# Optimization experiments

Measured on AMD Instinct MI355X. Metric: run time of the kernel, lower is better.

## Reference

```python
import jax, jax.numpy as jnp
import numpy as np

D_MODEL = 512
N_HEADS = 8
D_HEAD = D_MODEL // N_HEADS
D_FF = 2048
LN_EPS = 1e-5


def _layer_norm(x, g, b):
    mu = jnp.mean(x, axis=-1, keepdims=True)
    var = jnp.var(x, axis=-1, keepdims=True)
    return (x - mu) * jax.lax.rsqrt(var + LN_EPS) * g + b


def setup_inputs() -> dict:
    key = jax.random.key(0)
    ks = jax.random.split(key, 16)
    s_d = 1.0 / np.sqrt(D_MODEL)
    s_f = 1.0 / np.sqrt(D_FF)
    x = jax.random.normal(ks[0], (32, 512, D_MODEL), dtype=jnp.float32)
    # per-head Q/K/V linears stacked over heads: [H, D, dh] weights, [H, dh] biases
    Wq = jax.random.uniform(ks[1], (N_HEADS, D_MODEL, D_HEAD), jnp.float32, -s_d, s_d)
    bq = jax.random.uniform(ks[2], (N_HEADS, D_HEAD), jnp.float32, -s_d, s_d)
    Wk = jax.random.uniform(ks[3], (N_HEADS, D_MODEL, D_HEAD), jnp.float32, -s_d, s_d)
    bk = jax.random.uniform(ks[4], (N_HEADS, D_HEAD), jnp.float32, -s_d, s_d)
    Wv = jax.random.uniform(ks[5], (N_HEADS, D_MODEL, D_HEAD), jnp.float32, -s_d, s_d)
    bv = jax.random.uniform(ks[6], (N_HEADS, D_HEAD), jnp.float32, -s_d, s_d)
    Wo = jax.random.uniform(ks[7], (D_MODEL, D_MODEL), jnp.float32, -s_d, s_d)
    bo = jax.random.uniform(ks[8], (D_MODEL,), jnp.float32, -s_d, s_d)
    ln1_g = jnp.ones((D_MODEL,), jnp.float32)
    ln1_b = jnp.zeros((D_MODEL,), jnp.float32)
    W1 = jax.random.uniform(ks[9], (D_MODEL, D_FF), jnp.float32, -s_d, s_d)
    b1 = jax.random.uniform(ks[10], (D_FF,), jnp.float32, -s_d, s_d)
    W2 = jax.random.uniform(ks[11], (D_FF, D_MODEL), jnp.float32, -s_f, s_f)
    b2 = jax.random.uniform(ks[12], (D_MODEL,), jnp.float32, -s_f, s_f)
    ln2_g = jnp.ones((D_MODEL,), jnp.float32)
    ln2_b = jnp.zeros((D_MODEL,), jnp.float32)
    return dict(x=x, Wq=Wq, bq=bq, Wk=Wk, bk=bk, Wv=Wv, bv=bv, Wo=Wo, bo=bo,
                ln1_g=ln1_g, ln1_b=ln1_b, W1=W1, b1=b1, W2=W2, b2=b2,
                ln2_g=ln2_g, ln2_b=ln2_b)


def reference(x, Wq, bq, Wk, bk, Wv, bv, Wo, bo, ln1_g, ln1_b, W1, b1, W2, b2, ln2_g, ln2_b):
    B, T, D = x.shape
    # batched-heads Q/K/V: [B, H, T, dh]
    q = jnp.einsum('btd,hde->bhte', x, Wq) + bq[None, :, None, :]
    k = jnp.einsum('btd,hde->bhte', x, Wk) + bk[None, :, None, :]
    v = jnp.einsum('btd,hde->bhte', x, Wv) + bv[None, :, None, :]
    scale = D_HEAD ** -0.5
    scores = jnp.einsum('bhte,bhse->bhts', q, k) * scale  # [B,H,T,T]
    causal = jnp.tril(jnp.ones((T, T), dtype=bool))
    scores = jnp.where(causal[None, None], scores, -jnp.inf)
    w = jax.nn.softmax(scores, axis=-1)
    o = jnp.einsum('bhts,bhse->bhte', w, v)              # [B,H,T,dh]
    o = jnp.transpose(o, (0, 2, 1, 3)).reshape(B, T, D)   # concat heads
    attn = o @ Wo + bo
    out1 = x + _layer_norm(attn, ln1_g, ln1_b)            # post-LN on sublayer output (as in source)
    ff = jax.nn.relu(out1 @ W1 + b1) @ W2 + b2
    return out1 + _layer_norm(ff, ln2_g, ln2_b)
```

## Files before the change

### kernel.cpp

```cpp
#include <hip/hip_runtime.h>
#include <hip/hip_bf16.h>


#define D_MODEL 512
#define N_HEADS 8
#define D_HEAD 64
#define D_FF 2048
#define NROWS 16384

typedef __bf16 bf16x8 __attribute__((ext_vector_type(8)));
typedef float f32x4 __attribute__((ext_vector_type(4)));
typedef float f32x16 __attribute__((ext_vector_type(16)));

#define SWZ(x) ((x) ^ ((((x) >> 7) & 7) << 4))

static __device__ __forceinline__ ushort f2bf(float f) {
    union { float f; unsigned u; } v; v.f = f;
    unsigned r = v.u + 0x7fffu + ((v.u >> 16) & 1u);
    return (ushort)(r >> 16);
}
static __device__ __forceinline__ unsigned pack2(float lo, float hi) {
    return (unsigned)f2bf(lo) | ((unsigned)f2bf(hi) << 16);
}
static __device__ __forceinline__ void async16(const void* g, void* l) {
    __builtin_amdgcn_global_load_lds(
        (const __attribute__((address_space(1))) void*)g,
        (__attribute__((address_space(3))) void*)l, 16, 0, 0);
}

__global__ __launch_bounds__(256) void conv_bf_kernel(
    const float* __restrict__ src, ushort* __restrict__ dst, int n8)
{
    int i = blockIdx.x * 256 + threadIdx.x;
    if (i >= n8) return;
    const float4* s = (const float4*)src;
    float4 a = s[i * 2], b = s[i * 2 + 1];
    uint4 o;
    o.x = pack2(a.x, a.y); o.y = pack2(a.z, a.w);
    o.z = pack2(b.x, b.y); o.w = pack2(b.z, b.w);
    ((uint4*)dst)[i] = o;
}

static __device__ __forceinline__ void tile_transpose_body(
    const float* __restrict__ src, int srcldc, ushort* __restrict__ dst, int Rd,
    int r0, int c0)
{
    __shared__ float t[64][65];
    int tid = threadIdx.x;
    int lr = tid >> 4, lc4 = (tid & 15) * 4;
    #pragma unroll
    for (int i = 0; i < 4; ++i) {
        float4 v = *(const float4*)&src[(size_t)(r0 + lr + i * 16) * srcldc + c0 + lc4];
        t[lr + i * 16][lc4 + 0] = v.x;
        t[lr + i * 16][lc4 + 1] = v.y;
        t[lr + i * 16][lc4 + 2] = v.z;
        t[lr + i * 16][lc4 + 3] = v.w;
    }
    __syncthreads();
    int oc = tid >> 2, orr = (tid & 3) * 16;
    uint4 u0, u1;
    u0.x = pack2(t[orr + 0][oc],  t[orr + 1][oc]);
    u0.y = pack2(t[orr + 2][oc],  t[orr + 3][oc]);
    u0.z = pack2(t[orr + 4][oc],  t[orr + 5][oc]);
    u0.w = pack2(t[orr + 6][oc],  t[orr + 7][oc]);
    u1.x = pack2(t[orr + 8][oc],  t[orr + 9][oc]);
    u1.y = pack2(t[orr + 10][oc], t[orr + 11][oc]);
    u1.z = pack2(t[orr + 12][oc], t[orr + 13][oc]);
    u1.w = pack2(t[orr + 14][oc], t[orr + 15][oc]);
    ushort* d = dst + (size_t)(c0 + oc) * Rd + r0 + orr;
    *(uint4*)&d[0] = u0;
    *(uint4*)&d[8] = u1;
}

__global__ __launch_bounds__(256) void transpose_bf_kernel(
    const float* __restrict__ src, ushort* __restrict__ dst, int R, int C)
{
    tile_transpose_body(src, C, dst, R, blockIdx.y * 64, blockIdx.x * 64);
}

__global__ __launch_bounds__(256) void qkv_pack_kernel(
    const float* __restrict__ Wq, const float* __restrict__ Wk,
    const float* __restrict__ Wv, ushort* __restrict__ WpT)
{
    int z = blockIdx.z;
    int p = z >> 3, h = z & 7;
    const float* src = ((p == 0) ? Wq : (p == 1) ? Wk : Wv) + (size_t)h * D_MODEL * D_HEAD;
    ushort* dst = WpT + (size_t)(p * D_MODEL + h * D_HEAD) * D_MODEL;
    tile_transpose_body(src, D_HEAD, dst, D_MODEL, blockIdx.y * 64, 0);
}

__global__ __launch_bounds__(256) void pack_bias_kernel(
    const float* __restrict__ bq, const float* __restrict__ bk,
    const float* __restrict__ bv, float* __restrict__ bp)
{
    int idx = blockIdx.x * 256 + threadIdx.x;
    if (idx >= 3 * D_MODEL) return;
    int p = idx / D_MODEL;
    int h = (idx % D_MODEL) / D_HEAD;
    int e = idx % D_HEAD;
    const float* bb = (p == 0) ? bq : (p == 1) ? bk : bv;
    bp[idx] = bb[h * D_HEAD + e];
}

template<int OMODE, bool RELU>
__global__ __launch_bounds__(512, 1) void gemm_bf16_kernel(
    const ushort* __restrict__ A, const ushort* __restrict__ BT,
    const float* __restrict__ bias, void* __restrict__ Cout,
    ushort* __restrict__ Qg, ushort* __restrict__ Kg, ushort* __restrict__ Vt,
    int M, int N, int K, int nbx)
{
    extern __shared__ __align__(16) char smem[];

    const int tid = threadIdx.x;
    const int wid = tid >> 6, l = tid & 63;
    const int wr = wid >> 1, wc = wid & 1;

    const int total = gridDim.x;
    const int cpx = total >> 3;
    const int flat = blockIdx.x;
    const int swz = (flat & 7) * cpx + (flat >> 3);
    const int bx = swz % nbx, by = swz / nbx;
    const int m0 = by * 256, n0 = bx * 128;

    const int srow = tid >> 3;
    const int sbyte = (tid & 7) * 16;
    const int ssw = sbyte ^ ((srow & 7) << 4);

    #define STAGE(t)                                                          \
    {                                                                         \
        const int kk_ = (t) * 64;                                             \
        char* dst_ = smem + ((t) & 1) * 49152;                                \
        _Pragma("unroll")                                                     \
        for (int i = 0; i < 4; ++i)                                           \
            async16((const char*)(A + (size_t)(m0 + i * 64 + srow) * K + kk_) \
                        + ssw,                                                \
                    dst_ + i * 8192 + tid * 16);                              \
        _Pragma("unroll")                                                     \
        for (int i = 0; i < 2; ++i)                                           \
            async16((const char*)(BT + (size_t)(n0 + i * 64 + srow) * K + kk_)\
                        + ssw,                                                \
                    dst_ + 32768 + i * 8192 + tid * 16);                      \
    }

    const int fl = l & 31, fh = l >> 5;
    const int frsw = (fl & 7) << 4;

    f32x16 acc[2][2] = {};

    STAGE(0);
    const int T = K >> 6;
    for (int t = 0; t < T; ++t) {
        __builtin_amdgcn_s_barrier();
        if (t + 1 < T) {
            STAGE(t + 1);
            asm volatile("s_waitcnt vmcnt(6)" ::: "memory");
        } else {
            asm volatile("s_waitcnt vmcnt(0)" ::: "memory");
        }
        __builtin_amdgcn_sched_barrier(0);

        const char* bufA = smem + (t & 1) * 49152;
        const char* bufB = bufA + 32768;
        #pragma unroll
        for (int ks = 0; ks < 4; ++ks) {
            const int kb = ((ks * 32 + fh * 16) ^ frsw);
            bf16x8 af[2], bfv[2];
            #pragma unroll
            for (int mi = 0; mi < 2; ++mi)
                af[mi] = *(const bf16x8*)(bufA +
                    (wr * 64 + mi * 32 + fl) * 128 + kb);
            #pragma unroll
            for (int ni = 0; ni < 2; ++ni)
                bfv[ni] = *(const bf16x8*)(bufB +
                    (wc * 64 + ni * 32 + fl) * 128 + kb);
            #pragma unroll
            for (int mi = 0; mi < 2; ++mi)
                #pragma unroll
                for (int ni = 0; ni < 2; ++ni)
                    acc[mi][ni] = __builtin_amdgcn_mfma_f32_32x32x16_bf16(
                        af[mi], bfv[ni], acc[mi][ni], 0, 0, 0);
        }
    }

    #pragma unroll
    for (int ni = 0; ni < 2; ++ni) {
        const int c = n0 + wc * 64 + ni * 32 + fl;
        const float bvv = bias ? bias[c] : 0.f;
        #pragma unroll
        for (int mi = 0; mi < 2; ++mi) {
            const int rbase = m0 + wr * 64 + mi * 32 + (fh << 2);
            float vv[16];
            #pragma unroll
            for (int reg = 0; reg < 16; ++reg) {
                float v = acc[mi][ni][reg] + bvv;
                if (RELU) v = fmaxf(v, 0.f);
                vv[reg] = v;
            }
            if (OMODE == 0) {
                #pragma unroll
                for (int reg = 0; reg < 16; ++reg) {
                    int r = rbase + (reg & 3) + ((reg >> 2) << 3);
                    ((float*)Cout)[(size_t)r * N + c] = vv[reg];
                }
            } else if (OMODE == 1) {
                #pragma unroll
                for (int reg = 0; reg < 16; ++reg) {
                    int r = rbase + (reg & 3) + ((reg >> 2) << 3);
                    ((ushort*)Cout)[(size_t)r * N + c] = f2bf(vv[reg]);
                }
            } else {
                const int p = n0 >> 9;
                const int h = (c >> 6) & 7, e = c & 63;
                #pragma unroll
                for (int q = 0; q < 4; ++q) {
                    int r0 = rbase + (q << 3);
                    int b = r0 >> 9, t0 = r0 & 511;
                    size_t bh = (size_t)(b * 8 + h);
                    if (p == 2) {
                        uint2 pk;
                        pk.x = pack2(vv[q * 4 + 0], vv[q * 4 + 1]);
                        pk.y = pack2(vv[q * 4 + 2], vv[q * 4 + 3]);
                        *(uint2*)&Vt[bh * 32768 + (size_t)e * 512 + t0] = pk;
                    } else {
                        ushort* dst = (p == 0 ? Qg : Kg) + bh * 32768 +
                                      (size_t)t0 * 64 + e;
                        dst[0]   = f2bf(vv[q * 4 + 0]);
                        dst[64]  = f2bf(vv[q * 4 + 1]);
                        dst[128] = f2bf(vv[q * 4 + 2]);
                        dst[192] = f2bf(vv[q * 4 + 3]);
                    }
                }
            }
        }
    }
    #undef STAGE
}

__global__ __launch_bounds__(256) void attn_kernel(
    const ushort* __restrict__ Qg,
    const ushort* __restrict__ Kg,
    const ushort* __restrict__ Vt,
    ushort* __restrict__ O)
{
    __shared__ __align__(16) char QP[8192];
    __shared__ __align__(16) char KB[2][8192];
    __shared__ __align__(16) char VB[2][8192];

    const int bh = blockIdx.x, qb = blockIdx.y;
    const int tid = threadIdx.x;
    const int w = tid >> 6, l = tid & 63;

    const ushort* Qb = Qg + (size_t)bh * 32768;
    const ushort* Kb = Kg + (size_t)bh * 32768;
    const ushort* Vb = Vt + (size_t)bh * 32768;

    #pragma unroll
    for (int i = 0; i < 2; ++i) {
        int Xi = i * 4096 + tid * 16;
        int row = Xi >> 7;
        int sw = SWZ(Xi) & 127;
        async16((const char*)(Qb + (size_t)(qb * 64 + row) * 64) + sw, QP + Xi);
    }
    #define STAGEKV(kt, bb)                                                     \
        { _Pragma("unroll")                                                     \
          for (int i = 0; i < 2; ++i) {                                         \
              int Xi = i * 4096 + tid * 16;                                     \
              int row = Xi >> 7;                                                \
              int sw = SWZ(Xi) & 127;                                           \
              async16((const char*)(Kb + (size_t)((kt) * 64 + row) * 64) + sw,  \
                      KB[bb] + Xi);                                             \
              async16((const char*)(Vb + (size_t)row * 512 + (kt) * 64) + sw,   \
                      VB[bb] + Xi);                                             \
          } }
    STAGEKV(0, 0);
    __syncthreads();

    bf16x8 qf[2];
    {
        int qrow = w * 16 + (l & 15);
        #pragma unroll
        for (int ks = 0; ks < 2; ++ks) {
            int X = qrow * 128 + ks * 64 + (l >> 4) * 16;
            qf[ks] = *(const bf16x8*)(QP + SWZ(X));
        }
    }

    float mrow = -INFINITY, lrow = 0.f;
    f32x4 oacc[4] = {};

    for (int kt = 0; kt <= qb; ++kt) {
        int cur = kt & 1;
        if (kt < qb) STAGEKV(kt + 1, cur ^ 1);

        f32x4 sacc[4] = {};
        #pragma unroll
        for (int ks = 0; ks < 2; ++ks) {
            #pragma unroll
            for (int mi = 0; mi < 4; ++mi) {
                int X = (mi * 16 + (l & 15)) * 128 + ks * 64 + (l >> 4) * 16;
                bf16x8 kf = *(const bf16x8*)(KB[cur] + SWZ(X));
                sacc[mi] = __builtin_amdgcn_mfma_f32_16x16x32_bf16(
                    kf, qf[ks], sacc[mi], 0, 0, 0);
            }
        }

        float sv[16];
        float tmax = -INFINITY;
        const int qrow_t = w * 16 + (l & 15);
        #pragma unroll
        for (int mi = 0; mi < 4; ++mi)
            #pragma unroll
            for (int r = 0; r < 4; ++r) {
                float s = sacc[mi][r] * 0.125f;
                if (kt == qb) {
                    int key_l = mi * 16 + (l >> 4) * 4 + r;
                    if (key_l > qrow_t) s = -INFINITY;
                }
                sv[mi * 4 + r] = s;
                tmax = fmaxf(tmax, s);
            }
        tmax = fmaxf(tmax, __shfl_xor(tmax, 16));
        tmax = fmaxf(tmax, __shfl_xor(tmax, 32));
        float mnew = fmaxf(mrow, tmax);
        float corr = __expf(mrow - mnew);
        mrow = mnew;
        float psum = 0.f;
        #pragma unroll
        for (int i = 0; i < 16; ++i) { sv[i] = __expf(sv[i] - mnew); psum += sv[i]; }
        psum += __shfl_xor(psum, 16);
        psum += __shfl_xor(psum, 32);
        lrow = lrow * corr + psum;

        #pragma unroll
        for (int mi = 0; mi < 4; ++mi) {
            uint2 pk;
            pk.x = pack2(sv[mi * 4 + 0], sv[mi * 4 + 1]);
            pk.y = pack2(sv[mi * 4 + 2], sv[mi * 4 + 3]);
            int X = qrow_t * 128 + (mi * 16 + (l >> 4) * 4) * 2;
            *(uint2*)(QP + SWZ(X)) = pk;
        }

        #pragma unroll
        for (int r = 0; r < 4; ++r) {
            float cr = __shfl(corr, (l & 48) | ((l >> 4) * 4 + r));
            #pragma unroll
            for (int n = 0; n < 4; ++n) oacc[n][r] *= cr;
        }

        #pragma unroll
        for (int ks = 0; ks < 2; ++ks) {
            int Xa = qrow_t * 128 + ks * 64 + (l >> 4) * 16;
            bf16x8 pa = *(const bf16x8*)(QP + SWZ(Xa));
            #pragma unroll
            for (int n = 0; n < 4; ++n) {
                int Xb = (n * 16 + (l & 15)) * 128 + ks * 64 + (l >> 4) * 16;
                bf16x8 vb = *(const bf16x8*)(VB[cur] + SWZ(Xb));
                oacc[n] = __builtin_amdgcn_mfma_f32_16x16x32_bf16(
                    pa, vb, oacc[n], 0, 0, 0);
            }
        }
        __syncthreads();
    }

    float linv = 1.0f / lrow;
    const int b_ = bh >> 3, h_ = bh & 7;
    #pragma unroll
    for (int r = 0; r < 4; ++r) {
        float li = __shfl(linv, (l & 48) | ((l >> 4) * 4 + r));
        int trow = qb * 64 + w * 16 + (l >> 4) * 4 + r;
        size_t obase = ((size_t)b_ * 512 + trow) * 512 + h_ * 64 + (l & 15);
        #pragma unroll
        for (int n = 0; n < 4; ++n)
            O[obase + n * 16] = f2bf(oacc[n][r] * li);
    }
}

template<bool WBF>
__global__ __launch_bounds__(256) void ln_res_kernel(
    const float* __restrict__ v, const float* __restrict__ res,
    const float* __restrict__ g, const float* __restrict__ bb,
    float* __restrict__ out, ushort* __restrict__ out_bf)
{
    int row  = blockIdx.x * 4 + (threadIdx.x >> 6);
    int lane = threadIdx.x & 63;
    const float4* vp = (const float4*)(v + (size_t)row * D_MODEL);
    float4 a = vp[lane];
    float4 c = vp[lane + 64];
    float sum = a.x + a.y + a.z + a.w + c.x + c.y + c.z + c.w;
    float sq  = a.x*a.x + a.y*a.y + a.z*a.z + a.w*a.w
              + c.x*c.x + c.y*c.y + c.z*c.z + c.w*c.w;
    #pragma unroll
    for (int o = 1; o < 64; o <<= 1) {
        sum += __shfl_xor(sum, o);
        sq  += __shfl_xor(sq, o);
    }
    float mu   = sum * (1.f / 512.f);
    float var  = sq * (1.f / 512.f) - mu * mu;
    float rstd = rsqrtf(var + 1e-5f);

    const float4* rp = (const float4*)(res + (size_t)row * D_MODEL);
    const float4* gp = (const float4*)g;
    const float4* bp = (const float4*)bb;
    float4 r0 = rp[lane], r1 = rp[lane + 64];
    float4 g0 = gp[lane], g1 = gp[lane + 64];
    float4 b0 = bp[lane], b1 = bp[lane + 64];
    float4 o0, o1;
    o0.x = r0.x + (a.x - mu) * rstd * g0.x + b0.x;
    o0.y = r0.y + (a.y - mu) * rstd * g0.y + b0.y;
    o0.z = r0.z + (a.z - mu) * rstd * g0.z + b0.z;
    o0.w = r0.w + (a.w - mu) * rstd * g0.w + b0.w;
    o1.x = r1.x + (c.x - mu) * rstd * g1.x + b1.x;
    o1.y = r1.y + (c.y - mu) * rstd * g1.y + b1.y;
    o1.z = r1.z + (c.z - mu) * rstd * g1.z + b1.z;
    o1.w = r1.w + (c.w - mu) * rstd * g1.w + b1.w;
    float4* op = (float4*)(out + (size_t)row * D_MODEL);
    op[lane] = o0;
    op[lane + 64] = o1;
    if (WBF) {
        uint2 p0, p1;
        p0.x = pack2(o0.x, o0.y); p0.y = pack2(o0.z, o0.w);
        p1.x = pack2(o1.x, o1.y); p1.y = pack2(o1.z, o1.w);
        *(uint2*)&out_bf[(size_t)row * D_MODEL + lane * 4] = p0;
        *(uint2*)&out_bf[(size_t)row * D_MODEL + 256 + lane * 4] = p1;
    }
}

extern "C" void kernel_launch(void* const* d_in, const int* in_sizes, int n_in,
                              void* d_out, int out_size, void* d_ws, size_t ws_size,
                              hipStream_t stream)
{
    const float* x     = (const float*)d_in[0];
    const float* Wq    = (const float*)d_in[1];
    const float* bq    = (const float*)d_in[2];
    const float* Wk    = (const float*)d_in[3];
    const float* bk    = (const float*)d_in[4];
    const float* Wv    = (const float*)d_in[5];
    const float* bv    = (const float*)d_in[6];
    const float* Wo    = (const float*)d_in[7];
    const float* bo    = (const float*)d_in[8];
    const float* ln1_g = (const float*)d_in[9];
    const float* ln1_b = (const float*)d_in[10];
    const float* W1    = (const float*)d_in[11];
    const float* b1    = (const float*)d_in[12];
    const float* W2    = (const float*)d_in[13];
    const float* b2    = (const float*)d_in[14];
    const float* ln2_g = (const float*)d_in[15];
    const float* ln2_b = (const float*)d_in[16];

    float* ws = (float*)d_ws;
    ushort* Qg      = (ushort*)(ws);
    ushort* Kg      = (ushort*)(ws + 4194304);
    ushort* Vt      = (ushort*)(ws + 8388608);
    ushort* O_bf    = (ushort*)(ws + 12582912);
    float*  attnb   = ws + 16777216;
    float*  out1    = ws + 25165824;
    ushort* out1_bf = (ushort*)(ws + 33554432);
    ushort* x_bf    = (ushort*)(ws + 37748736);
    ushort* WpT     = (ushort*)(ws + 41943040);
    ushort* WoT     = (ushort*)(ws + 42336256);
    ushort* W1T     = (ushort*)(ws + 42467328);
    ushort* W2T     = (ushort*)(ws + 42991616);
    float*  bp      = ws + 43515904;
    ushort* ff1_bf  = (ushort*)ws;
    float*  ff2     = attnb;

    (void)hipFuncSetAttribute(
        reinterpret_cast<const void*>(&gemm_bf16_kernel<2, false>),
        hipFuncAttributeMaxDynamicSharedMemorySize, 98304);
    (void)hipFuncSetAttribute(
        reinterpret_cast<const void*>(&gemm_bf16_kernel<0, false>),
        hipFuncAttributeMaxDynamicSharedMemorySize, 98304);
    (void)hipFuncSetAttribute(
        reinterpret_cast<const void*>(&gemm_bf16_kernel<1, true>),
        hipFuncAttributeMaxDynamicSharedMemorySize, 98304);

    conv_bf_kernel<<<dim3(4096), 256, 0, stream>>>(x, x_bf, NROWS * D_MODEL / 8);
    qkv_pack_kernel<<<dim3(1, 8, 24), 256, 0, stream>>>(Wq, Wk, Wv, WpT);
    transpose_bf_kernel<<<dim3(8, 8), 256, 0, stream>>>(Wo, WoT, 512, 512);
    transpose_bf_kernel<<<dim3(32, 8), 256, 0, stream>>>(W1, W1T, 512, 2048);
    transpose_bf_kernel<<<dim3(8, 32), 256, 0, stream>>>(W2, W2T, 2048, 512);
    pack_bias_kernel<<<dim3(6), 256, 0, stream>>>(bq, bk, bv, bp);

    gemm_bf16_kernel<2, false><<<dim3(768), 512, 98304, stream>>>(
        x_bf, WpT, bp, nullptr, Qg, Kg, Vt, NROWS, 1536, 512, 12);

    attn_kernel<<<dim3(256, 8), 256, 0, stream>>>(Qg, Kg, Vt, O_bf);

    gemm_bf16_kernel<0, false><<<dim3(256), 512, 98304, stream>>>(
        O_bf, WoT, bo, attnb, nullptr, nullptr, nullptr, NROWS, 512, 512, 4);

    ln_res_kernel<true><<<dim3(NROWS / 4), 256, 0, stream>>>(
        attnb, x, ln1_g, ln1_b, out1, out1_bf);

    gemm_bf16_kernel<1, true><<<dim3(1024), 512, 98304, stream>>>(
        out1_bf, W1T, b1, ff1_bf, nullptr, nullptr, nullptr, NROWS, 2048, 512, 16);

    gemm_bf16_kernel<0, false><<<dim3(256), 512, 98304, stream>>>(
        ff1_bf, W2T, b2, ff2, nullptr, nullptr, nullptr, NROWS, 512, 2048, 4);

    ln_res_kernel<false><<<dim3(NROWS / 4), 256, 0, stream>>>(
        ff2, out1, ln2_g, ln2_b, (float*)d_out, nullptr);
}
```

Measured before the change: 224.0 us.

## Enlarge GEMM tiles to 256x256 with 4-stage 32-wide K pipeline

The bf16 GEMM now computes 256x256 output tiles per block, with each wave holding a 128x64 sub-tile, instead of 256x128. The K loop steps by 32 through a 4-buffer LDS ring with two tiles of prefetch, uses a new XOR swizzle, and raises wave priority around the MFMA bursts. The goal is to cut LDS and global traffic per FLOP and hide load latency better. In exchange it uses more accumulator registers and 128KB of LDS, and it halves the grid size, which may leave CUs idle for the smaller N=512 GEMMs (128 blocks).

```diff
diff --git a/kernel.cpp b/kernel.cpp
--- a/kernel.cpp
+++ b/kernel.cpp
@@ -103,7 +103,7 @@
 }
 
 template<int OMODE, bool RELU>
-__global__ __launch_bounds__(512, 1) void gemm_bf16_kernel(
+__global__ __launch_bounds__(512, 2) void gemm_bf16_kernel(
     const ushort* __restrict__ A, const ushort* __restrict__ BT,
     const float* __restrict__ bias, void* __restrict__ Cout,
     ushort* __restrict__ Qg, ushort* __restrict__ Kg, ushort* __restrict__ Vt,
@@ -113,82 +113,83 @@
 
     const int tid = threadIdx.x;
     const int wid = tid >> 6, l = tid & 63;
-    const int wr = wid >> 1, wc = wid & 1;
-
-    const int total = gridDim.x;
-    const int cpx = total >> 3;
+    const int wm = wid >> 2, wn = wid & 3;
+
+    const int cpx = gridDim.x >> 3;
     const int flat = blockIdx.x;
     const int swz = (flat & 7) * cpx + (flat >> 3);
     const int bx = swz % nbx, by = swz / nbx;
-    const int m0 = by * 256, n0 = bx * 128;
-
-    const int srow = tid >> 3;
-    const int sbyte = (tid & 7) * 16;
-    const int ssw = sbyte ^ ((srow & 7) << 4);
-
-    #define STAGE(t)                                                          \
-    {                                                                         \
-        const int kk_ = (t) * 64;                                             \
-        char* dst_ = smem + ((t) & 1) * 49152;                                \
-        _Pragma("unroll")                                                     \
-        for (int i = 0; i < 4; ++i)                                           \
-            async16((const char*)(A + (size_t)(m0 + i * 64 + srow) * K + kk_) \
-                        + ssw,                                                \
-                    dst_ + i * 8192 + tid * 16);                              \
-        _Pragma("unroll")                                                     \
-        for (int i = 0; i < 2; ++i)                                           \
-            async16((const char*)(BT + (size_t)(n0 + i * 64 + srow) * K + kk_)\
-                        + ssw,                                                \
-                    dst_ + 32768 + i * 8192 + tid * 16);                      \
+    const int m0 = by * 256, n0 = bx * 256;
+
+    const int T = K >> 5;
+
+    #define STAGE(t)                                                           \
+    if ((t) < T) {                                                             \
+        char* dst_ = smem + ((t) & 3) * 32768;                                 \
+        const int kb0_ = (t) * 64;                                             \
+        _Pragma("unroll")                                                      \
+        for (int i = 0; i < 2; ++i) {                                          \
+            int X = i * 8192 + tid * 16;                                       \
+            int row = X >> 6;                                                  \
+            int kb = (X & 63) ^ ((row & 3) << 4);                              \
+            async16((const char*)A + (size_t)(m0 + row) * (K * 2) + kb0_ + kb, \
+                    dst_ + X);                                                 \
+            async16((const char*)BT + (size_t)(n0 + row) * (K * 2) + kb0_ + kb,\
+                    dst_ + 16384 + X);                                         \
+        }                                                                      \
     }
 
     const int fl = l & 31, fh = l >> 5;
-    const int frsw = (fl & 7) << 4;
-
-    f32x16 acc[2][2] = {};
+    const int swl = (fl & 3) << 4;
+
+    f32x16 acc[4][2] = {};
 
     STAGE(0);
-    const int T = K >> 6;
-    for (int t = 0; t < T; ++t) {
-        __builtin_amdgcn_s_barrier();
-        if (t + 1 < T) {
-            STAGE(t + 1);
-            asm volatile("s_waitcnt vmcnt(6)" ::: "memory");
-        } else {
-            asm volatile("s_waitcnt vmcnt(0)" ::: "memory");
-        }
-        __builtin_amdgcn_sched_barrier(0);
-
-        const char* bufA = smem + (t & 1) * 49152;
-        const char* bufB = bufA + 32768;
-        #pragma unroll
-        for (int ks = 0; ks < 4; ++ks) {
-            const int kb = ((ks * 32 + fh * 16) ^ frsw);
-            bf16x8 af[2], bfv[2];
-            #pragma unroll
-            for (int mi = 0; mi < 2; ++mi)
-                af[mi] = *(const bf16x8*)(bufA +
-                    (wr * 64 + mi * 32 + fl) * 128 + kb);
+    STAGE(1);
+    if (T > 1) asm volatile("s_waitcnt vmcnt(4)" ::: "memory");
+    else       asm volatile("s_waitcnt vmcnt(0)" ::: "memory");
+    __builtin_amdgcn_s_barrier();
+    __builtin_amdgcn_sched_barrier(0);
+
+    for (int kt = 0; kt < T; ++kt) {
+        STAGE(kt + 2);
+
+        const char* bA = smem + (kt & 3) * 32768 + (wm * 128 + fl) * 64;
+        const char* bB = smem + (kt & 3) * 32768 + 16384 + (wn * 64 + fl) * 64;
+        #pragma unroll
+        for (int ks = 0; ks < 2; ++ks) {
+            const int kb = (ks * 32 + fh * 16) ^ swl;
+            bf16x8 af[4], bfv[2];
+            #pragma unroll
+            for (int mi = 0; mi < 4; ++mi)
+                af[mi] = *(const bf16x8*)(bA + mi * 2048 + kb);
             #pragma unroll
             for (int ni = 0; ni < 2; ++ni)
-                bfv[ni] = *(const bf16x8*)(bufB +
-                    (wc * 64 + ni * 32 + fl) * 128 + kb);
-            #pragma unroll
-            for (int mi = 0; mi < 2; ++mi)
+                bfv[ni] = *(const bf16x8*)(bB + ni * 2048 + kb);
+            __builtin_amdgcn_s_setprio(1);
+            #pragma unroll
+            for (int mi = 0; mi < 4; ++mi)
                 #pragma unroll
                 for (int ni = 0; ni < 2; ++ni)
                     acc[mi][ni] = __builtin_amdgcn_mfma_f32_32x32x16_bf16(
                         af[mi], bfv[ni], acc[mi][ni], 0, 0, 0);
-        }
-    }
+            __builtin_amdgcn_s_setprio(0);
+        }
+
+        if (kt < T - 2) asm volatile("s_waitcnt vmcnt(4)" ::: "memory");
+        else            asm volatile("s_waitcnt vmcnt(0)" ::: "memory");
+        __builtin_amdgcn_s_barrier();
+        __builtin_amdgcn_sched_barrier(0);
+    }
+    #undef STAGE
 
     #pragma unroll
     for (int ni = 0; ni < 2; ++ni) {
-        const int c = n0 + wc * 64 + ni * 32 + fl;
+        const int c = n0 + wn * 64 + ni * 32 + fl;
         const float bvv = bias ? bias[c] : 0.f;
         #pragma unroll
-        for (int mi = 0; mi < 2; ++mi) {
-            const int rbase = m0 + wr * 64 + mi * 32 + (fh << 2);
+        for (int mi = 0; mi < 4; ++mi) {
+            const int rbase = m0 + wm * 128 + mi * 32 + (fh << 2);
             float vv[16];
             #pragma unroll
             for (int reg = 0; reg < 16; ++reg) {
@@ -233,7 +234,6 @@
             }
         }
     }
-    #undef STAGE
 }
 
 __global__ __launch_bounds__(256) void attn_kernel(
@@ -466,13 +466,13 @@
 
     (void)hipFuncSetAttribute(
         reinterpret_cast<const void*>(&gemm_bf16_kernel<2, false>),
-        hipFuncAttributeMaxDynamicSharedMemorySize, 98304);
+        hipFuncAttributeMaxDynamicSharedMemorySize, 131072);
     (void)hipFuncSetAttribute(
         reinterpret_cast<const void*>(&gemm_bf16_kernel<0, false>),
-        hipFuncAttributeMaxDynamicSharedMemorySize, 98304);
+        hipFuncAttributeMaxDynamicSharedMemorySize, 131072);
     (void)hipFuncSetAttribute(
         reinterpret_cast<const void*>(&gemm_bf16_kernel<1, true>),
-        hipFuncAttributeMaxDynamicSharedMemorySize, 98304);
+        hipFuncAttributeMaxDynamicSharedMemorySize, 131072);
 
     conv_bf_kernel<<<dim3(4096), 256, 0, stream>>>(x, x_bf, NROWS * D_MODEL / 8);
     qkv_pack_kernel<<<dim3(1, 8, 24), 256, 0, stream>>>(Wq, Wk, Wv, WpT);
@@ -481,22 +481,22 @@
     transpose_bf_kernel<<<dim3(8, 32), 256, 0, stream>>>(W2, W2T, 2048, 512);
     pack_bias_kernel<<<dim3(6), 256, 0, stream>>>(bq, bk, bv, bp);
 
-    gemm_bf16_kernel<2, false><<<dim3(768), 512, 98304, stream>>>(
-        x_bf, WpT, bp, nullptr, Qg, Kg, Vt, NROWS, 1536, 512, 12);
+    gemm_bf16_kernel<2, false><<<dim3(384), 512, 131072, stream>>>(
+        x_bf, WpT, bp, nullptr, Qg, Kg, Vt, NROWS, 1536, 512, 6);
 
     attn_kernel<<<dim3(256, 8), 256, 0, stream>>>(Qg, Kg, Vt, O_bf);
 
-    gemm_bf16_kernel<0, false><<<dim3(256), 512, 98304, stream>>>(
-        O_bf, WoT, bo, attnb, nullptr, nullptr, nullptr, NROWS, 512, 512, 4);
+    gemm_bf16_kernel<0, false><<<dim3(128), 512, 131072, stream>>>(
+        O_bf, WoT, bo, attnb, nullptr, nullptr, nullptr, NROWS, 512, 512, 2);
 
     ln_res_kernel<true><<<dim3(NROWS / 4), 256, 0, stream>>>(
         attnb, x, ln1_g, ln1_b, out1, out1_bf);
 
-    gemm_bf16_kernel<1, true><<<dim3(1024), 512, 98304, stream>>>(
-        out1_bf, W1T, b1, ff1_bf, nullptr, nullptr, nullptr, NROWS, 2048, 512, 16);
-
-    gemm_bf16_kernel<0, false><<<dim3(256), 512, 98304, stream>>>(
-        ff1_bf, W2T, b2, ff2, nullptr, nullptr, nullptr, NROWS, 512, 2048, 4);
+    gemm_bf16_kernel<1, true><<<dim3(512), 512, 131072, stream>>>(
+        out1_bf, W1T, b1, ff1_bf, nullptr, nullptr, nullptr, NROWS, 2048, 512, 8);
+
+    gemm_bf16_kernel<0, false><<<dim3(128), 512, 131072, stream>>>(
+        ff1_bf, W2T, b2, ff2, nullptr, nullptr, nullptr, NROWS, 512, 2048, 2);
 
     ln_res_kernel<false><<<dim3(NROWS / 4), 256, 0, stream>>>(
         ff2, out1, ln2_g, ln2_b, (float*)d_out, nullptr);
```

Result: slower. 278.1 us (+24.2%).
